# Performance work log

Measured on AMD Instinct MI355X. Metric: run time of the kernel, lower is better.

Reference implementation:

```python
import jax, jax.numpy as jnp
import numpy as np

N_NODES = 50000
N_EDGES = 1_600_000
D = 64


def setup_inputs() -> dict:
    key = jax.random.key(0)
    k1, k2, k3, k4 = jax.random.split(key, 4)
    x = jax.random.normal(k1, (N_NODES, D), dtype=jnp.float32)
    # Glorot-ish scale for the dense transform
    weight = jax.random.normal(k2, (D, D), dtype=jnp.float32) * (1.0 / np.sqrt(D))
    bias = jnp.zeros((D,), dtype=jnp.float32)
    src = jax.random.randint(k3, (N_EDGES,), 0, N_NODES, dtype=jnp.int32)
    dst = jax.random.randint(k4, (N_EDGES,), 0, N_NODES, dtype=jnp.int32)
    t = jnp.zeros((1,), dtype=jnp.float32)
    return {"t": t, "x": x, "weight": weight, "bias": bias, "src": src, "dst": dst}


def reference(t, x, weight, bias, src, dst):
    # GCDEFunc.forward(t, x) -> GCNLayer(x); dropout=0 (eval / ODE solve).
    n = x.shape[0]
    # symmetric GCN normalization: 1/sqrt(in_degree), 0 for isolated nodes
    deg = jax.ops.segment_sum(jnp.ones_like(dst, dtype=x.dtype), dst, num_segments=n)
    norm = jnp.where(deg > 0, jax.lax.rsqrt(jnp.maximum(deg, 1.0)), 0.0)[:, None]  # [N,1]
    h = x @ weight                 # [N,D] dense transform
    h = h * norm                   # src-side normalization
    # SpMM: sum messages copy_src(h) over incoming edges
    h = jax.ops.segment_sum(h[src], dst, num_segments=n)  # [N,D]
    h = h * norm + bias            # dst-side normalization + bias
    return jax.nn.softplus(h)      # smooth activation for ODE dynamics
```

## Files before the change

### kernel.cpp

```cpp
#include <hip/hip_runtime.h>
#include <hip/hip_fp16.h>

constexpr int N = 50000;
constexpr int D = 64;
constexpr int E = 1600000;
constexpr int NBUCK = (N + 127) / 128;
constexpr int CAP = 4608;
constexpr int BTHREADS = 512;
constexpr int CPT = 8;
constexpr int EPB = BTHREADS * CPT;
constexpr int BUCK_BLOCKS = (E + EPB - 1) / EPB;

__global__ void k_init(int* __restrict__ cursor) {
    int t = threadIdx.x;
    if (t < NBUCK) cursor[t] = t * CAP;
}

__global__ void k_bucket(const int* __restrict__ src, const int* __restrict__ dst,
                         int* __restrict__ cursor, unsigned* __restrict__ packed) {
    __shared__ int lh[NBUCK];
    __shared__ int scan[BTHREADS];
    __shared__ int lb[NBUCK];
    __shared__ unsigned stage[EPB];
    int tid = threadIdx.x;
    for (int i = tid; i < NBUCK; i += BTHREADS) lh[i] = 0;
    __syncthreads();
    int base_e = blockIdx.x * EPB;
    unsigned pk[CPT];
    int bn[CPT], rk[CPT];
#pragma unroll
    for (int i = 0; i < CPT; ++i) {
        int e = base_e + i * BTHREADS + tid;
        if (e < E) {
            int d = dst[e];
            int s = src[e];
            bn[i] = d >> 7;
            pk[i] = ((unsigned)d << 16) | (unsigned)s;
            rk[i] = atomicAdd(&lh[bn[i]], 1);
        } else bn[i] = -1;
    }
    __syncthreads();
    scan[tid] = (tid < NBUCK) ? lh[tid] : 0;
    __syncthreads();
    for (int off = 1; off < BTHREADS; off <<= 1) {
        int v = (tid >= off) ? scan[tid - off] : 0;
        __syncthreads();
        scan[tid] += v;
        __syncthreads();
    }
    if (tid < NBUCK) {
        int c = lh[tid];
        lb[tid] = c ? atomicAdd(&cursor[tid], c) : 0;
    }
    __syncthreads();
#pragma unroll
    for (int i = 0; i < CPT; ++i) {
        if (bn[i] >= 0) {
            int eb = (bn[i] == 0) ? 0 : scan[bn[i] - 1];
            stage[eb + rk[i]] = pk[i];
        }
    }
    __syncthreads();
    int tot = scan[NBUCK - 1];
    for (int j = tid; j < tot; j += BTHREADS) {
        unsigned v = stage[j];
        int bk = v >> 23;
        int eb = (bk == 0) ? 0 : scan[bk - 1];
        packed[lb[bk] + (j - eb)] = v;
    }
}

__global__ void k_csr(const int* __restrict__ cursor, const unsigned* __restrict__ packed,
                      unsigned short* __restrict__ csr, int* __restrict__ rowptr,
                      int* __restrict__ rowend, float* __restrict__ norm) {
    __shared__ int cnt[128];
    __shared__ int sm[128];
    __shared__ int cur[128];
    __shared__ unsigned short stage[CAP];
    int b = blockIdx.x, tid = threadIdx.x;
    if (tid < 128) cnt[tid] = 0;
    __syncthreads();
    int beg = b * CAP;
    int m = cursor[b] - beg;
    for (int j = tid; j < m; j += 512)
        atomicAdd(&cnt[(packed[beg + j] >> 16) & 127], 1);
    __syncthreads();
    if (tid < 128) sm[tid] = cnt[tid];
    __syncthreads();
    for (int off = 1; off < 128; off <<= 1) {
        int v = 0;
        if (tid < 128 && tid >= off) v = sm[tid - off];
        __syncthreads();
        if (tid < 128) sm[tid] += v;
        __syncthreads();
    }
    if (tid < 128) {
        int excl = (tid == 0) ? 0 : sm[tid - 1];
        int node = b * 128 + tid;
        if (node < N) {
            rowptr[node] = beg + excl;
            rowend[node] = beg + sm[tid];
            norm[node] = cnt[tid] ? rsqrtf((float)cnt[tid]) : 0.0f;
        }
        cur[tid] = excl;
    }
    __syncthreads();
    for (int j = tid; j < m; j += 512) {
        unsigned p = packed[beg + j];
        int slot = atomicAdd(&cur[(p >> 16) & 127], 1);
        stage[slot] = (unsigned short)(p & 0xFFFFu);
    }
    __syncthreads();
    unsigned* du = (unsigned*)(csr + beg);
    const unsigned* su = (const unsigned*)stage;
    int mu = m >> 1;
    for (int k = tid; k < mu; k += 512) du[k] = su[k];
    if ((m & 1) && tid == 0) csr[beg + m - 1] = stage[m - 1];
}

__global__ void k_gemm(const float* __restrict__ x, const float* __restrict__ W,
                       const float* __restrict__ norm, __half* __restrict__ h2) {
    __shared__ float Wl[64 * 64];
    __shared__ float xs[16][64];
    int tid = threadIdx.x;
    const float4* W4 = (const float4*)W;
    float4* Wl4 = (float4*)Wl;
    Wl4[tid] = W4[tid];
    int r = tid >> 6, d = tid & 63;
    int row = blockIdx.x * 16 + r;
    xs[r][d] = x[row * 64 + d];
    __syncthreads();
    float a = 0.0f;
#pragma unroll
    for (int k = 0; k < 64; ++k) a = fmaf(xs[r][k], Wl[k * 64 + d], a);
    h2[row * 64 + d] = __float2half(a * norm[row]);
}

__global__ void k_aggregate(const int* __restrict__ rowptr, const int* __restrict__ rowend,
                            const unsigned short* __restrict__ csr,
                            const __half* __restrict__ h2, const float* __restrict__ norm,
                            const float* __restrict__ bias, float* __restrict__ out) {
    int node = blockIdx.x * 4 + (threadIdx.x >> 6);
    int lane = threadIdx.x & 63;
    int half = lane >> 5;
    int fl = lane & 31;
    const __half2* h2v = (const __half2*)h2;
    int beg = rowptr[node];
    int end = rowend[node];
    float ax = 0.0f, ay = 0.0f, bx = 0.0f, by = 0.0f;
    int j = beg;
    for (; j + 7 < end; j += 8) {
        int s0 = csr[j + half];
        int s1 = csr[j + 2 + half];
        int s2 = csr[j + 4 + half];
        int s3 = csr[j + 6 + half];
        float2 v0 = __half22float2(h2v[s0 * 32 + fl]);
        float2 v1 = __half22float2(h2v[s1 * 32 + fl]);
        float2 v2 = __half22float2(h2v[s2 * 32 + fl]);
        float2 v3 = __half22float2(h2v[s3 * 32 + fl]);
        ax += v0.x + v2.x;  ay += v0.y + v2.y;
        bx += v1.x + v3.x;  by += v1.y + v3.y;
    }
    for (; j + 1 < end; j += 2) {
        int s = csr[j + half];
        float2 v = __half22float2(h2v[s * 32 + fl]);
        ax += v.x;  ay += v.y;
    }
    if (j < end && half == 0) {
        int s = csr[j];
        float2 v = __half22float2(h2v[s * 32 + fl]);
        ax += v.x;  ay += v.y;
    }
    ax += bx;  ay += by;
    ax += __shfl_xor(ax, 32, 64);
    ay += __shfl_xor(ay, 32, 64);
    if (half == 0) {
        float nrm = norm[node];
        float2 bs = ((const float2*)bias)[fl];
        float vx = ax * nrm + bs.x;
        float vy = ay * nrm + bs.y;
        float2 o;
        o.x = fmaxf(vx, 0.0f) + log1pf(expf(-fabsf(vx)));
        o.y = fmaxf(vy, 0.0f) + log1pf(expf(-fabsf(vy)));
        ((float2*)out)[node * 32 + fl] = o;
    }
}

extern "C" void kernel_launch(void* const* d_in, const int* in_sizes, int n_in,
                              void* d_out, int out_size, void* d_ws, size_t ws_size,
                              hipStream_t stream) {
    const float* x    = (const float*)d_in[1];
    const float* W    = (const float*)d_in[2];
    const float* bias = (const float*)d_in[3];
    const int* src = (const int*)d_in[4];
    const int* dst = (const int*)d_in[5];
    float* out = (float*)d_out;

    char* ws = (char*)d_ws;
    __half*         h2     = (__half*)(ws);
    unsigned*       packed = (unsigned*)(ws + 6400000);
    unsigned short* csr    = (unsigned short*)(ws + 13606912);
    int*            rowptr = (int*)(ws + 17210368);
    int*            rowend = (int*)(ws + 17410368);
    float*          norm   = (float*)(ws + 17610368);
    int*            cursor = (int*)(ws + 17810368);

    k_init     <<<1, 512, 0, stream>>>(cursor);
    k_bucket   <<<BUCK_BLOCKS, BTHREADS, 0, stream>>>(src, dst, cursor, packed);
    k_csr      <<<NBUCK, 512, 0, stream>>>(cursor, packed, csr, rowptr, rowend, norm);
    k_gemm     <<<(N + 15) / 16, 1024, 0, stream>>>(x, W, norm, h2);
    k_aggregate<<<(N + 3) / 4, 256, 0, stream>>>(rowptr, rowend, csr, h2, norm, bias, out);
}
```

Baseline: 165.9 us.

## Split h2 into feature-half planes and map planes to XCD groups in aggregate

```diff
diff --git a/kernel.cpp b/kernel.cpp
--- a/kernel.cpp
+++ b/kernel.cpp
@@ -133,56 +133,56 @@
     float a = 0.0f;
 #pragma unroll
     for (int k = 0; k < 64; ++k) a = fmaf(xs[r][k], Wl[k * 64 + d], a);
-    h2[row * 64 + d] = __float2half(a * norm[row]);
+    h2[(size_t)(d >> 5) * (N * 32) + row * 32 + (d & 31)] = __float2half(a * norm[row]);
 }
 
 __global__ void k_aggregate(const int* __restrict__ rowptr, const int* __restrict__ rowend,
                             const unsigned short* __restrict__ csr,
                             const __half* __restrict__ h2, const float* __restrict__ norm,
                             const float* __restrict__ bias, float* __restrict__ out) {
-    int node = blockIdx.x * 4 + (threadIdx.x >> 6);
+    int xcd = blockIdx.x & 7;
+    int plane = xcd >> 2;
+    int o = (blockIdx.x >> 3) * 4 + (xcd & 3);
+    int node = o * 4 + (threadIdx.x >> 6);
     int lane = threadIdx.x & 63;
-    int half = lane >> 5;
-    int fl = lane & 31;
-    const __half2* h2v = (const __half2*)h2;
+    int q = lane >> 4;
+    int fl = lane & 15;
+    const __half2* h2v = (const __half2*)(h2 + (size_t)plane * (N * 32));
     int beg = rowptr[node];
     int end = rowend[node];
     float ax = 0.0f, ay = 0.0f, bx = 0.0f, by = 0.0f;
     int j = beg;
     for (; j + 7 < end; j += 8) {
-        int s0 = csr[j + half];
-        int s1 = csr[j + 2 + half];
-        int s2 = csr[j + 4 + half];
-        int s3 = csr[j + 6 + half];
-        float2 v0 = __half22float2(h2v[s0 * 32 + fl]);
-        float2 v1 = __half22float2(h2v[s1 * 32 + fl]);
-        float2 v2 = __half22float2(h2v[s2 * 32 + fl]);
-        float2 v3 = __half22float2(h2v[s3 * 32 + fl]);
-        ax += v0.x + v2.x;  ay += v0.y + v2.y;
-        bx += v1.x + v3.x;  by += v1.y + v3.y;
-    }
-    for (; j + 1 < end; j += 2) {
-        int s = csr[j + half];
-        float2 v = __half22float2(h2v[s * 32 + fl]);
+        int s0 = csr[j + q];
+        int s1 = csr[j + 4 + q];
+        float2 v0 = __half22float2(h2v[s0 * 16 + fl]);
+        float2 v1 = __half22float2(h2v[s1 * 16 + fl]);
+        ax += v0.x;  ay += v0.y;
+        bx += v1.x;  by += v1.y;
+    }
+    for (; j + 3 < end; j += 4) {
+        int s = csr[j + q];
+        float2 v = __half22float2(h2v[s * 16 + fl]);
         ax += v.x;  ay += v.y;
     }
-    if (j < end && half == 0) {
-        int s = csr[j];
-        float2 v = __half22float2(h2v[s * 32 + fl]);
-        ax += v.x;  ay += v.y;
+    if (j < end) {
+        bool act = (j + q) < end;
+        int s = csr[act ? (j + q) : beg];
+        float2 v = __half22float2(h2v[s * 16 + fl]);
+        if (act) { ax += v.x;  ay += v.y; }
     }
     ax += bx;  ay += by;
-    ax += __shfl_xor(ax, 32, 64);
-    ay += __shfl_xor(ay, 32, 64);
-    if (half == 0) {
+    ax += __shfl_xor(ax, 16, 64);  ay += __shfl_xor(ay, 16, 64);
+    ax += __shfl_xor(ax, 32, 64);  ay += __shfl_xor(ay, 32, 64);
+    if (q == 0) {
         float nrm = norm[node];
-        float2 bs = ((const float2*)bias)[fl];
+        float2 bs = ((const float2*)bias)[plane * 16 + fl];
         float vx = ax * nrm + bs.x;
         float vy = ay * nrm + bs.y;
-        float2 o;
-        o.x = fmaxf(vx, 0.0f) + log1pf(expf(-fabsf(vx)));
-        o.y = fmaxf(vy, 0.0f) + log1pf(expf(-fabsf(vy)));
-        ((float2*)out)[node * 32 + fl] = o;
+        float2 o2;
+        o2.x = fmaxf(vx, 0.0f) + log1pf(expf(-fabsf(vx)));
+        o2.y = fmaxf(vy, 0.0f) + log1pf(expf(-fabsf(vy)));
+        ((float2*)out)[node * 32 + plane * 16 + fl] = o2;
     }
 }
 
@@ -209,5 +209,5 @@
     k_bucket   <<<BUCK_BLOCKS, BTHREADS, 0, stream>>>(src, dst, cursor, packed);
     k_csr      <<<NBUCK, 512, 0, stream>>>(cursor, packed, csr, rowptr, rowend, norm);
     k_gemm     <<<(N + 15) / 16, 1024, 0, stream>>>(x, W, norm, h2);
-    k_aggregate<<<(N + 3) / 4, 256, 0, stream>>>(rowptr, rowend, csr, h2, norm, bias, out);
-}
+    k_aggregate<<<25000, 256, 0, stream>>>(rowptr, rowend, csr, h2, norm, bias, out);
+}
```

After: 186.7 us. 1.13x slower.
